# Kernel tuning notes

Measured on AMD Instinct MI355X. Metric: run time of the kernel, lower is better.

## Reference

```python
import jax, jax.numpy as jnp
import numpy as np

B, C, L = 8, 512, 2048


def setup_inputs() -> dict:
    key = jax.random.key(0)
    ks = jax.random.split(key, 7)
    s = 1.0 / np.sqrt(C)
    return {
        "x": jax.random.normal(ks[0], (B, C, L), dtype=jnp.float32),
        "Wq": jax.random.normal(ks[1], (C, C), dtype=jnp.float32) * s,
        "bq": jax.random.normal(ks[2], (C,), dtype=jnp.float32) * s,
        "Wk": jax.random.normal(ks[3], (C, C), dtype=jnp.float32) * s,
        "bk": jax.random.normal(ks[4], (C,), dtype=jnp.float32) * s,
        "Wv": jax.random.normal(ks[5], (C, C), dtype=jnp.float32) * s,
        "bv": jax.random.normal(ks[6], (C,), dtype=jnp.float32) * s,
    }


def reference(x, Wq, bq, Wk, bk, Wv, bv):
    # Conv1d(kernel_size=1) == per-position linear: [C_out, C_in] @ x[b,:,l]
    q = jnp.einsum('oi,bil->bol', Wq, x) + bq[None, :, None]  # [B, C, L]
    k = jnp.einsum('oi,bil->bol', Wk, x) + bk[None, :, None]
    v = jnp.einsum('oi,bil->bol', Wv, x) + bv[None, :, None]
    scale = 1.0 / jnp.sqrt(jnp.asarray(x.shape[1], dtype=x.dtype))
    # scores[b, l, m] = sum_c q[b,c,l] * k[b,c,m] / sqrt(C)
    scores = jnp.einsum('bcl,bcm->blm', q, k) * scale  # [B, L, L]
    attn = jax.nn.softmax(scores, axis=-1)
    # out[b, c, l] = sum_m v[b,c,m] * attn[b,l,m]   (== bmm(V, attn^T))
    return jnp.einsum('bcm,blm->bcl', v, attn)  # [B, C, L]
```

## Files before the change

### kernel.cpp

```cpp
#include <hip/hip_runtime.h>
#include <hip/hip_bf16.h>
#include <math.h>

#define B 8
#define C 512
#define L 2048

using bf16x8 = __bf16 __attribute__((ext_vector_type(8)));
using f32x4  = float __attribute__((ext_vector_type(4)));

#define MFMA(a, b, c) __builtin_amdgcn_mfma_f32_16x16x32_bf16((a), (b), (c), 0, 0, 0)
#define SC2 0.06375872f
#define SH2 -17.312340f
#define MEMFENCE() asm volatile("" ::: "memory")
#define BAR()  do { MEMFENCE(); __builtin_amdgcn_s_barrier(); MEMFENCE(); } while (0)
#define LGKM0() do { asm volatile("s_waitcnt lgkmcnt(0)" ::: "memory"); \
                     __builtin_amdgcn_sched_barrier(0); } while (0)

__device__ __forceinline__ unsigned short f2bf(float f) {
    unsigned int u; __builtin_memcpy(&u, &f, 4);
    u += 0x7FFF + ((u >> 16) & 1);
    return (unsigned short)(u >> 16);
}
__device__ __forceinline__ void load_lds16(const unsigned short* g, unsigned short* l) {
    __builtin_amdgcn_global_load_lds(
        (const __attribute__((address_space(1))) unsigned int*)g,
        (__attribute__((address_space(3))) unsigned int*)l, 16, 0, 0);
}
__device__ __forceinline__ bf16x8 dsr128(unsigned byteoff) {
    bf16x8 r;
    asm volatile("ds_read_b128 %0, %1" : "=v"(r) : "v"(byteoff));
    return r;
}

template<int MODE, int KDIM>
__device__ __forceinline__ void gemm_core(
    const unsigned short* __restrict__ A,
    const unsigned short* __restrict__ Bm,
    unsigned short* As, unsigned short* Bs,
    void* __restrict__ OutV, int ldo,
    float* __restrict__ ep)
{
    const int t = threadIdx.x;
    const int wave = t >> 6, lane = t & 63;
    const int ll = t & 15, quad = (t >> 4) & 3;
    const int lr = lane >> 2, chunk = lane & 3;
    const int wm = (wave & 1) * 64, wn = (wave >> 1) * 64;

    const unsigned short* gA0 = A  + (size_t)(wave * 32 + lr) * KDIM + chunk * 8;
    const unsigned short* gB0 = Bm + (size_t)(wave * 32 + lr) * KDIM + chunk * 8;
    unsigned short* lA0 = As + (wave * 32) * 32;
    unsigned short* lB0 = Bs + (wave * 32) * 32;
    const int P1 = 128 * 32;

    f32x4 acc[4][4];
#pragma unroll
    for (int i = 0; i < 4; ++i)
#pragma unroll
        for (int j = 0; j < 4; ++j) acc[i][j] = (f32x4){0.f, 0.f, 0.f, 0.f};

#pragma unroll 1
    for (int k0 = 0; k0 < KDIM; k0 += 64) {
        __syncthreads();
        load_lds16(gA0 + k0, lA0);
        load_lds16(gA0 + (size_t)16 * KDIM + k0, lA0 + 16 * 32);
        load_lds16(gA0 + k0 + 32, lA0 + P1);
        load_lds16(gA0 + (size_t)16 * KDIM + k0 + 32, lA0 + P1 + 16 * 32);
        load_lds16(gB0 + k0, lB0);
        load_lds16(gB0 + (size_t)16 * KDIM + k0, lB0 + 16 * 32);
        load_lds16(gB0 + k0 + 32, lB0 + P1);
        load_lds16(gB0 + (size_t)16 * KDIM + k0 + 32, lB0 + P1 + 16 * 32);
        __syncthreads();

#pragma unroll
        for (int p = 0; p < 2; ++p) {
            bf16x8 af[4], bf[4];
#pragma unroll
            for (int mi = 0; mi < 4; ++mi)
                af[mi] = *(const bf16x8*)&As[p * P1 + (wm + mi * 16 + ll) * 32 + quad * 8];
#pragma unroll
            for (int ni = 0; ni < 4; ++ni)
                bf[ni] = *(const bf16x8*)&Bs[p * P1 + (wn + ni * 16 + ll) * 32 + quad * 8];
#pragma unroll
            for (int mi = 0; mi < 4; ++mi)
#pragma unroll
                for (int ni = 0; ni < 4; ++ni)
                    acc[mi][ni] = MFMA(af[mi], bf[ni], acc[mi][ni]);
        }
    }

#pragma unroll
    for (int mi = 0; mi < 4; ++mi)
#pragma unroll
        for (int ni = 0; ni < 4; ++ni) {
            const int col = wn + ni * 16 + ll;
            float epc = 0.f;
            if (MODE == 0) epc = ep[col];
            if (MODE == 3) epc = 1.0f / ep[col];
#pragma unroll
            for (int r = 0; r < 4; ++r) {
                const int row = wm + mi * 16 + quad * 4 + r;
                float v = acc[mi][ni][r];
                if (MODE == 0)      v += epc;
                else if (MODE == 1) v += ep[row];
                else                v *= epc;
                if (MODE == 3)
                    ((float*)OutV)[(size_t)row * ldo + col] = v;
                else
                    ((unsigned short*)OutV)[(size_t)row * ldo + col] = f2bf(v);
            }
        }
}

__global__ __launch_bounds__(256) void xpose_cvt(
    const float* __restrict__ x, unsigned short* __restrict__ xt)
{
    __shared__ float tile[64][69];
    const int b = blockIdx.z, l0 = blockIdx.x * 64, c0 = blockIdx.y * 64;
    const int t = threadIdx.x;
    const int lx = t & 15, cy = t >> 4;
    const float* xb = x + (size_t)b * C * L;
#pragma unroll
    for (int p = 0; p < 4; ++p) {
        float4 v = *(const float4*)(xb + (size_t)(c0 + p * 16 + cy) * L + l0 + lx * 4);
        tile[p * 16 + cy][lx * 4 + 0] = v.x;
        tile[p * 16 + cy][lx * 4 + 1] = v.y;
        tile[p * 16 + cy][lx * 4 + 2] = v.z;
        tile[p * 16 + cy][lx * 4 + 3] = v.w;
    }
    __syncthreads();
    const int ocl = t & 15, ot = t >> 4;
    unsigned short* xtb = xt + (size_t)b * L * C;
#pragma unroll
    for (int p = 0; p < 4; ++p) {
        int ol = p * 16 + ot;
        union { unsigned short h[4]; uint2 u; } pk;
#pragma unroll
        for (int i = 0; i < 4; ++i) pk.h[i] = f2bf(tile[ocl * 4 + i][ol]);
        *(uint2*)(xtb + (size_t)(l0 + ol) * C + c0 + ocl * 4) = pk.u;
    }
}

__global__ __launch_bounds__(256) void wcvt(
    const float* __restrict__ Wq, const float* __restrict__ Wk,
    const float* __restrict__ Wv, unsigned short* __restrict__ o,
    float* __restrict__ rsum)
{
    if (blockIdx.x < 16) {
        float4 z = make_float4(0.f, 0.f, 0.f, 0.f);
        *(float4*)(rsum + (blockIdx.x * 256 + threadIdx.x) * 4) = z;
    }
    const int i = (blockIdx.x * 256 + threadIdx.x) * 4;
    const int which = i >> 18;
    const int off = i & 0x3FFFF;
    const float* src = (which == 0) ? Wq : (which == 1) ? Wk : Wv;
    float4 v = *(const float4*)(src + off);
    union { unsigned short h[4]; uint2 u; } pk;
    pk.h[0] = f2bf(v.x); pk.h[1] = f2bf(v.y); pk.h[2] = f2bf(v.z); pk.h[3] = f2bf(v.w);
    *(uint2*)(o + i) = pk.u;
}

__global__ __launch_bounds__(256) void qkv_gemm(
    const unsigned short* __restrict__ xt, const unsigned short* __restrict__ Wb,
    const float* __restrict__ bq, const float* __restrict__ bk,
    const float* __restrict__ bv,
    unsigned short* __restrict__ Qt, unsigned short* __restrict__ Kt,
    unsigned short* __restrict__ Vv)
{
    __shared__ unsigned short As[2 * 128 * 32], Bs[2 * 128 * 32];
    const int id = blockIdx.x;
    const int b = id & 7, r = id >> 3;
    const int which = r >> 6, tt = r & 63;
    const unsigned short* xtb = xt + (size_t)b * L * C;
    if (which < 2) {
        const int m0 = (tt & 15) * 128, n0 = (tt >> 4) * 128;
        const unsigned short* A  = xtb + (size_t)m0 * C;
        const unsigned short* Bm = Wb + (size_t)which * C * C + (size_t)n0 * C;
        unsigned short* Out = (which ? Kt : Qt) + (size_t)b * L * C
                              + (size_t)m0 * C + n0;
        gemm_core<0, C>(A, Bm, As, Bs, Out, C,
                        const_cast<float*>((which ? bk : bq) + n0));
    } else {
        const int m0 = (tt & 3) * 128, n0 = (tt >> 2) * 128;
        const unsigned short* A  = Wb + (size_t)2 * C * C + (size_t)m0 * C;
        const unsigned short* Bm = xtb + (size_t)n0 * C;
        unsigned short* Out = Vv + (size_t)b * C * L + (size_t)m0 * L + n0;
        gemm_core<1, C>(A, Bm, As, Bs, Out, L, const_cast<float*>(bv + m0));
    }
}

__global__ __launch_bounds__(512, 2) void sc_exp2(
    const unsigned short* __restrict__ Qt, const unsigned short* __restrict__ Kt,
    unsigned short* __restrict__ P, float* __restrict__ rsum,
    int hoff, int qrows, int mshift)
{
    __shared__ unsigned short As[2][16384], Bs[2][16384];
    constexpr int KD = C;
    constexpr int NT = C / 64;

    const int id = blockIdx.x;
    const int b = id & 7, rr = id >> 3;
    const int m0 = (rr & ((1 << mshift) - 1)) * 256, n0 = (rr >> mshift) * 256;
    const unsigned short* A  = Qt + (size_t)b * L * C + (size_t)(hoff + m0) * C;
    const unsigned short* Bm = Kt + (size_t)b * L * C + (size_t)n0 * C;
    unsigned short* Out = P + (size_t)b * qrows * L + (size_t)m0 * L + n0;
    float* ep = rsum + (size_t)b * L + hoff + m0;

    const int t = threadIdx.x;
    const int wave = t >> 6, lane = t & 63;
    const int ll = lane & 15, quad = lane >> 4;
    const int wm = wave & 1, wn = wave >> 1;
    const int r0 = t >> 3;
    const int swz = ((t & 7) ^ (r0 & 7)) * 8;
    const int sw8 = ll & 7;
    const unsigned c0b = (unsigned)(((quad ^ sw8)) * 16);
    const unsigned c1b = (unsigned)((((4 + quad) ^ sw8)) * 16);
    const unsigned aBb = (unsigned)(wm * 16384 + ll * 128);
    const unsigned bBb = (unsigned)(wn * 8192  + ll * 128);
    const unsigned ldsA = (unsigned)(unsigned long long)&As[0][0];
    const unsigned ldsB = (unsigned)(unsigned long long)&Bs[0][0];

    const unsigned short* gA = A  + (size_t)r0 * KD + swz;
    const unsigned short* gB = Bm + (size_t)r0 * KD + swz;

    f32x4 acc[8][4];
#pragma unroll
    for (int i = 0; i < 8; ++i)
#pragma unroll
        for (int j = 0; j < 4; ++j) acc[i][j] = (f32x4){0.f, 0.f, 0.f, 0.f};

    {
        unsigned short* sA0 = &As[0][0] + wave * 512;
        unsigned short* sB0 = &Bs[0][0] + wave * 512;
        unsigned short* sB1 = &Bs[1][0] + wave * 512;
        load_lds16(gA,                          sA0);
        load_lds16(gA + (size_t)64  * KD,       sA0 + 4096);
        load_lds16(gA + (size_t)128 * KD,       sA0 + 8192);
        load_lds16(gA + (size_t)192 * KD,       sA0 + 12288);
        load_lds16(gB,                          sB0);
        load_lds16(gB + (size_t)64  * KD,       sB0 + 4096);
        load_lds16(gB + (size_t)128 * KD,       sB0 + 8192);
        load_lds16(gB + (size_t)192 * KD,       sB0 + 12288);
        load_lds16(gB + 64,                     sB1);
        load_lds16(gB + (size_t)64  * KD + 64,  sB1 + 4096);
        load_lds16(gB + (size_t)128 * KD + 64,  sB1 + 8192);
        load_lds16(gB + (size_t)192 * KD + 64,  sB1 + 12288);
        asm volatile("s_waitcnt vmcnt(4)" ::: "memory");
        __builtin_amdgcn_sched_barrier(0);
        BAR();
    }

#define CLUSTER(base)                                                          \
    __builtin_amdgcn_s_setprio(1);                                             \
    _Pragma("unroll")                                                          \
    for (int mi2 = 0; mi2 < 2; ++mi2)                                          \
        _Pragma("unroll")                                                      \
        for (int ni = 0; ni < 4; ++ni) {                                       \
            acc[(base) + mi2][ni] = MFMA(af[mi2][0], bfr[ni][0], acc[(base) + mi2][ni]); \
            acc[(base) + mi2][ni] = MFMA(af[mi2][1], bfr[ni][1], acc[(base) + mi2][ni]); \
        }                                                                      \
    __builtin_amdgcn_s_setprio(0);

#pragma unroll 1
    for (int kt = 0; kt < NT; ++kt) {
        const int p = kt & 1;
        const unsigned aAdr = ldsA + (unsigned)(p * 32768) + aBb;
        const unsigned bAdr = ldsB + (unsigned)(p * 32768) + bBb;
        const int kaOff = (kt + 1 < NT ? kt + 1 : 0) * 64;
        const int kbOff = (kt + 2 < NT ? kt + 2 : 0) * 64;
        unsigned short* stA = &As[(kt + 1) & 1][0] + wave * 512;
        unsigned short* stB = &Bs[p][0] + wave * 512;

        bf16x8 bfr[4][2], af[2][2];

#pragma unroll
        for (int ni = 0; ni < 4; ++ni) {
            bfr[ni][0] = dsr128(bAdr + ni * 2048 + c0b);
            bfr[ni][1] = dsr128(bAdr + ni * 2048 + c1b);
        }
        af[0][0] = dsr128(aAdr + 0 * 2048 + c0b);
        af[0][1] = dsr128(aAdr + 0 * 2048 + c1b);
        af[1][0] = dsr128(aAdr + 1 * 2048 + c0b);
        af[1][1] = dsr128(aAdr + 1 * 2048 + c1b);
        load_lds16(gA + kaOff,                    stA);
        load_lds16(gA + (size_t)64 * KD + kaOff,  stA + 4096);
        BAR();
        LGKM0();
        CLUSTER(0);
        BAR();

        af[0][0] = dsr128(aAdr + 2 * 2048 + c0b);
        af[0][1] = dsr128(aAdr + 2 * 2048 + c1b);
        af[1][0] = dsr128(aAdr + 3 * 2048 + c0b);
        af[1][1] = dsr128(aAdr + 3 * 2048 + c1b);
        load_lds16(gA + (size_t)128 * KD + kaOff, stA + 8192);
        load_lds16(gA + (size_t)192 * KD + kaOff, stA + 12288);
        BAR();
        LGKM0();
        CLUSTER(2);
        BAR();

        af[0][0] = dsr128(aAdr + 4 * 2048 + c0b);
        af[0][1] = dsr128(aAdr + 4 * 2048 + c1b);
        af[1][0] = dsr128(aAdr + 5 * 2048 + c0b);
        af[1][1] = dsr128(aAdr + 5 * 2048 + c1b);
        load_lds16(gB + kbOff,                    stB);
        load_lds16(gB + (size_t)64 * KD + kbOff,  stB + 4096);
        BAR();
        LGKM0();
        CLUSTER(4);
        BAR();

        af[0][0] = dsr128(aAdr + 6 * 2048 + c0b);
        af[0][1] = dsr128(aAdr + 6 * 2048 + c1b);
        af[1][0] = dsr128(aAdr + 7 * 2048 + c0b);
        af[1][1] = dsr128(aAdr + 7 * 2048 + c1b);
        load_lds16(gB + (size_t)128 * KD + kbOff, stB + 8192);
        load_lds16(gB + (size_t)192 * KD + kbOff, stB + 12288);
        BAR();
        LGKM0();
        CLUSTER(6);
        asm volatile("s_waitcnt vmcnt(4)" ::: "memory");
        __builtin_amdgcn_sched_barrier(0);
        BAR();
    }
#undef CLUSTER

    float rpart[8][4];
#pragma unroll
    for (int mi = 0; mi < 8; ++mi)
#pragma unroll
        for (int r = 0; r < 4; ++r) rpart[mi][r] = 0.f;

#pragma unroll
    for (int mi = 0; mi < 8; ++mi)
#pragma unroll
        for (int ni = 0; ni < 4; ++ni) {
            const int col = wn * 64 + ni * 16 + ll;
#pragma unroll
            for (int r = 0; r < 4; ++r) {
                const int row = wm * 128 + mi * 16 + quad * 4 + r;
                float v = exp2f(fmaf(acc[mi][ni][r], SC2, SH2));
                rpart[mi][r] += v;
                Out[(size_t)row * L + col] = f2bf(v);
            }
        }
#pragma unroll
    for (int mi = 0; mi < 8; ++mi)
#pragma unroll
        for (int r = 0; r < 4; ++r) {
            float s = rpart[mi][r];
            s += __shfl_xor(s, 1, 64);
            s += __shfl_xor(s, 2, 64);
            s += __shfl_xor(s, 4, 64);
            s += __shfl_xor(s, 8, 64);
            if (ll == 0) atomicAdd(ep + wm * 128 + mi * 16 + quad * 4 + r, s);
        }
}

__global__ __launch_bounds__(256) void pv_gemm(
    const unsigned short* __restrict__ Vv, const unsigned short* __restrict__ P,
    const float* __restrict__ rsum, float* __restrict__ out,
    int hoff, int qrows)
{
    __shared__ unsigned short As[2 * 128 * 32], Bs[2 * 128 * 32];
    const int id = blockIdx.x;
    const int b = id & 7, r = id >> 3;
    const int m0 = (r & 3) * 128, n0 = (r >> 2) * 128;
    const unsigned short* A  = Vv + (size_t)b * C * L + (size_t)m0 * L;
    const unsigned short* Bm = P + (size_t)b * qrows * L + (size_t)n0 * L;
    float* Out = out + (size_t)b * C * L + (size_t)m0 * L + hoff + n0;
    float* ep = const_cast<float*>(rsum) + (size_t)b * L + hoff + n0;
    gemm_core<3, L>(A, Bm, As, Bs, Out, L, ep);
}

extern "C" void kernel_launch(void* const* d_in, const int* in_sizes, int n_in,
                              void* d_out, int out_size, void* d_ws, size_t ws_size,
                              hipStream_t stream) {
    const float* x  = (const float*)d_in[0];
    const float* Wq = (const float*)d_in[1];
    const float* bq = (const float*)d_in[2];
    const float* Wk = (const float*)d_in[3];
    const float* bk = (const float*)d_in[4];
    const float* Wv = (const float*)d_in[5];
    const float* bv = (const float*)d_in[6];
    float* out = (float*)d_out;

    const size_t BCL = (size_t)B * C * L;
    const bool fullP = ws_size >= 119078912ull;

    unsigned short* Qt = (unsigned short*)d_ws;
    unsigned short* Kt = Qt + BCL;
    unsigned short* Vv = Kt + BCL;
    unsigned short *Wb, *xt, *P;
    float* rsum;
    if (fullP) {
        Wb   = Vv + BCL;
        rsum = (float*)(Wb + (size_t)3 * C * C);
        xt   = (unsigned short*)(rsum + (size_t)B * L);
        P    = xt;
    } else {
        xt   = Vv + BCL;
        P    = xt;
        Wb   = P + (size_t)B * 1024 * L;
        rsum = (float*)(Wb + (size_t)3 * C * C);
    }

    xpose_cvt<<<dim3(L / 64, C / 64, B), 256, 0, stream>>>(x, xt);
    wcvt<<<dim3(3 * C * C / 1024), 256, 0, stream>>>(Wq, Wk, Wv, Wb, rsum);
    qkv_gemm<<<dim3(1536), 256, 0, stream>>>(xt, Wb, bq, bk, bv, Qt, Kt, Vv);

    if (fullP) {
        sc_exp2<<<dim3(512), 512, 0, stream>>>(Qt, Kt, P, rsum, 0, L, 3);
        pv_gemm<<<dim3(512), 256, 0, stream>>>(Vv, P, rsum, out, 0, L);
    } else {
        for (int h = 0; h < 2; ++h) {
            sc_exp2<<<dim3(256), 512, 0, stream>>>(Qt, Kt, P, rsum, h * 1024, 1024, 2);
            pv_gemm<<<dim3(256), 256, 0, stream>>>(Vv, P, rsum, out, h * 1024, 1024);
        }
    }
}
```

Baseline: 234.2 us.

## Double-buffer A fragments in registers and cut barriers in the GEMM main loop

Restructures the main K-loop so that A fragments ping-pong between two register sets (afA/afB). The LDS reads for the next cluster are issued before the current cluster's MFMAs, using partial lgkmcnt waits instead of full waits. Workgroup barriers per iteration drop from eight to two, and global-to-LDS prefetches are moved earlier. The aim is to hide LDS latency and barrier stalls behind MFMA work, at the cost of higher VGPR pressure and tighter reliance on the wait counts being exact.

```diff
diff --git a/kernel.cpp b/kernel.cpp
--- a/kernel.cpp
+++ b/kernel.cpp
@@ -14,8 +14,8 @@
 #define SH2 -17.312340f
 #define MEMFENCE() asm volatile("" ::: "memory")
 #define BAR()  do { MEMFENCE(); __builtin_amdgcn_s_barrier(); MEMFENCE(); } while (0)
-#define LGKM0() do { asm volatile("s_waitcnt lgkmcnt(0)" ::: "memory"); \
-                     __builtin_amdgcn_sched_barrier(0); } while (0)
+#define LGKMC(n) do { asm volatile("s_waitcnt lgkmcnt(" #n ")" ::: "memory"); \
+                      __builtin_amdgcn_sched_barrier(0); } while (0)
 
 __device__ __forceinline__ unsigned short f2bf(float f) {
     unsigned int u; __builtin_memcpy(&u, &f, 4);
@@ -250,14 +250,14 @@
         BAR();
     }
 
-#define CLUSTER(base)                                                          \
+#define CLUSTER(base, F)                                                       \
     __builtin_amdgcn_s_setprio(1);                                             \
     _Pragma("unroll")                                                          \
     for (int mi2 = 0; mi2 < 2; ++mi2)                                          \
         _Pragma("unroll")                                                      \
         for (int ni = 0; ni < 4; ++ni) {                                       \
-            acc[(base) + mi2][ni] = MFMA(af[mi2][0], bfr[ni][0], acc[(base) + mi2][ni]); \
-            acc[(base) + mi2][ni] = MFMA(af[mi2][1], bfr[ni][1], acc[(base) + mi2][ni]); \
+            acc[(base) + mi2][ni] = MFMA(F[mi2][0], bfr[ni][0], acc[(base) + mi2][ni]); \
+            acc[(base) + mi2][ni] = MFMA(F[mi2][1], bfr[ni][1], acc[(base) + mi2][ni]); \
         }                                                                      \
     __builtin_amdgcn_s_setprio(0);
 
@@ -271,55 +271,47 @@
         unsigned short* stA = &As[(kt + 1) & 1][0] + wave * 512;
         unsigned short* stB = &Bs[p][0] + wave * 512;
 
-        bf16x8 bfr[4][2], af[2][2];
-
+        bf16x8 bfr[4][2], afA[2][2], afB[2][2];
+
+        load_lds16(gA + kaOff,                    stA);
+        load_lds16(gA + (size_t)64 * KD + kaOff,  stA + 4096);
 #pragma unroll
         for (int ni = 0; ni < 4; ++ni) {
             bfr[ni][0] = dsr128(bAdr + ni * 2048 + c0b);
             bfr[ni][1] = dsr128(bAdr + ni * 2048 + c1b);
         }
-        af[0][0] = dsr128(aAdr + 0 * 2048 + c0b);
-        af[0][1] = dsr128(aAdr + 0 * 2048 + c1b);
-        af[1][0] = dsr128(aAdr + 1 * 2048 + c0b);
-        af[1][1] = dsr128(aAdr + 1 * 2048 + c1b);
-        load_lds16(gA + kaOff,                    stA);
-        load_lds16(gA + (size_t)64 * KD + kaOff,  stA + 4096);
-        BAR();
-        LGKM0();
-        CLUSTER(0);
-        BAR();
-
-        af[0][0] = dsr128(aAdr + 2 * 2048 + c0b);
-        af[0][1] = dsr128(aAdr + 2 * 2048 + c1b);
-        af[1][0] = dsr128(aAdr + 3 * 2048 + c0b);
-        af[1][1] = dsr128(aAdr + 3 * 2048 + c1b);
+        afA[0][0] = dsr128(aAdr + 0 * 2048 + c0b);
+        afA[0][1] = dsr128(aAdr + 0 * 2048 + c1b);
+        afA[1][0] = dsr128(aAdr + 1 * 2048 + c0b);
+        afA[1][1] = dsr128(aAdr + 1 * 2048 + c1b);
+        afB[0][0] = dsr128(aAdr + 2 * 2048 + c0b);
+        afB[0][1] = dsr128(aAdr + 2 * 2048 + c1b);
+        afB[1][0] = dsr128(aAdr + 3 * 2048 + c0b);
+        afB[1][1] = dsr128(aAdr + 3 * 2048 + c1b);
+        LGKMC(4);
+        CLUSTER(0, afA);
         load_lds16(gA + (size_t)128 * KD + kaOff, stA + 8192);
         load_lds16(gA + (size_t)192 * KD + kaOff, stA + 12288);
+        afA[0][0] = dsr128(aAdr + 4 * 2048 + c0b);
+        afA[0][1] = dsr128(aAdr + 4 * 2048 + c1b);
+        afA[1][0] = dsr128(aAdr + 5 * 2048 + c0b);
+        afA[1][1] = dsr128(aAdr + 5 * 2048 + c1b);
+        LGKMC(4);
+        CLUSTER(2, afB);
         BAR();
-        LGKM0();
-        CLUSTER(2);
-        BAR();
-
-        af[0][0] = dsr128(aAdr + 4 * 2048 + c0b);
-        af[0][1] = dsr128(aAdr + 4 * 2048 + c1b);
-        af[1][0] = dsr128(aAdr + 5 * 2048 + c0b);
-        af[1][1] = dsr128(aAdr + 5 * 2048 + c1b);
+
         load_lds16(gB + kbOff,                    stB);
         load_lds16(gB + (size_t)64 * KD + kbOff,  stB + 4096);
-        BAR();
-        LGKM0();
-        CLUSTER(4);
-        BAR();
-
-        af[0][0] = dsr128(aAdr + 6 * 2048 + c0b);
-        af[0][1] = dsr128(aAdr + 6 * 2048 + c1b);
-        af[1][0] = dsr128(aAdr + 7 * 2048 + c0b);
-        af[1][1] = dsr128(aAdr + 7 * 2048 + c1b);
+        afB[0][0] = dsr128(aAdr + 6 * 2048 + c0b);
+        afB[0][1] = dsr128(aAdr + 6 * 2048 + c1b);
+        afB[1][0] = dsr128(aAdr + 7 * 2048 + c0b);
+        afB[1][1] = dsr128(aAdr + 7 * 2048 + c1b);
+        LGKMC(4);
+        CLUSTER(4, afA);
         load_lds16(gB + (size_t)128 * KD + kbOff, stB + 8192);
         load_lds16(gB + (size_t)192 * KD + kbOff, stB + 12288);
-        BAR();
-        LGKM0();
-        CLUSTER(6);
+        LGKMC(0);
+        CLUSTER(6, afB);
         asm volatile("s_waitcnt vmcnt(4)" ::: "memory");
         __builtin_amdgcn_sched_barrier(0);
         BAR();
```

Measured after the change: 231.6 us. About the same (-1.1%).
